# Kernel optimization log

Measured on AMD Instinct MI355X. Metric: run time of the kernel, lower is better.

Reference implementation:

```python
import jax, jax.numpy as jnp
import numpy as np

N_NODES = 10000
N_EDGES = 100000
IN_FEATS = 64
OUT_FEATS = 64
N_EDGE_TYPES = 10


def setup_inputs() -> dict:
    key = jax.random.key(0)
    k_feat, k_src, k_dst, k_ord, k_emb = jax.random.split(key, 5)
    feat = jax.random.normal(k_feat, (N_NODES, IN_FEATS), dtype=jnp.float32)
    src = jax.random.randint(k_src, (N_EDGES,), 0, N_NODES, dtype=jnp.int32)
    dst = jax.random.randint(k_dst, (N_EDGES,), 0, N_NODES, dtype=jnp.int32)
    order = jax.random.randint(k_ord, (N_EDGES,), 0, N_EDGE_TYPES, dtype=jnp.int32)
    # xavier-uniform-like init for the relation-weight embedding table
    emb_weight = jax.random.normal(k_emb, (N_EDGE_TYPES, IN_FEATS * OUT_FEATS), dtype=jnp.float32) * 0.02
    bias = jnp.zeros((OUT_FEATS,), dtype=jnp.float32)
    return {"feat": feat, "src": src, "dst": dst, "order": order,
            "emb_weight": emb_weight, "bias": bias}


def reference(feat, src, dst, order, emb_weight, bias):
    n_nodes, in_feats = feat.shape
    out_feats = emb_weight.shape[1] // in_feats
    n_edges = src.shape[0]
    ones_e = jnp.ones((n_edges,), dtype=feat.dtype)

    # norm='both': scale source features by out_degree^{-1/2}
    out_deg = jnp.clip(jax.ops.segment_sum(ones_e, src, num_segments=n_nodes), 1.0)
    feat_n = feat * (out_deg ** -0.5)[:, None]

    # per-edge relation weight gather: [E, out, in]
    w = emb_weight[order].reshape(n_edges, out_feats, in_feats)
    h_src = feat_n[src]                              # [E, in]
    msg = jnp.einsum('eoi,ei->eo', w, h_src)         # [E, out]

    # scatter-sum aggregate to destination nodes
    rst = jax.ops.segment_sum(msg, dst, num_segments=n_nodes)  # [N, out]

    # post-norm by in_degree^{-1/2}
    in_deg = jnp.clip(jax.ops.segment_sum(ones_e, dst, num_segments=n_nodes), 1.0)
    rst = rst * (in_deg ** -0.5)[:, None]
    return rst + bias
```

## Files before the change

kernel.cpp:

```cpp
#include <hip/hip_runtime.h>
#include <stdint.h>


typedef __attribute__((ext_vector_type(8))) short short8;
typedef __attribute__((ext_vector_type(4))) float f32x4;

constexpr int N_NODES = 10000;
constexpr int N_EDGES = 100000;
constexpr int F = 64;
constexpr int R = 10;
constexpr int BLOCK = 256;
constexpr int CAPN = 64;
constexpr int WPR = (N_NODES + 31) / 32;
constexpr int GBX = (WPR + (BLOCK / 64) - 1) / (BLOCK / 64);

union U8 { uint32_t u[4]; short8 s; };

__device__ inline uint32_t pk_hi(float x, float y) {
    uint32_t bx = __float_as_uint(x), by = __float_as_uint(y);
    return (bx >> 16) | (by & 0xFFFF0000u);
}
__device__ inline uint32_t pk_lo(float x, float y) {
    uint32_t bx = __float_as_uint(x), by = __float_as_uint(y);
    float lx = x - __uint_as_float(bx & 0xFFFF0000u);
    float ly = y - __uint_as_float(by & 0xFFFF0000u);
    return (__float_as_uint(lx) >> 16) | (__float_as_uint(ly) & 0xFFFF0000u);
}

__global__ void k_count(const int* __restrict__ src, const int* __restrict__ dst,
                        const int* __restrict__ order, const float* __restrict__ emb,
                        const float* __restrict__ feat,
                        unsigned* deg_out, unsigned* deg_in,
                        const unsigned* __restrict__ sent_ptr,
                        uint4* __restrict__ wfrag, int* __restrict__ dstbuf,
                        uint4* __restrict__ pfeat) {
    unsigned sent = *sent_ptr;
    int t = blockIdx.x * BLOCK + threadIdx.x;

    if (t < N_EDGES) {
        int s = src[t], d = dst[t], r = order[t];
        atomicAdd(&deg_out[s], 1u);
        int rank = (int)(atomicAdd(&deg_in[d], 1u) - sent);
        if (rank < CAPN)
            dstbuf[d * CAPN + rank] = r * N_NODES + s;
    }

    if (t < R * 16 * 64) {
        int lane = t & 63, frag = t >> 6;
        int p = frag & 1, ks = (frag >> 1) & 1, tt = (frag >> 2) & 3, rr = frag >> 4;
        int o = 16 * tt + (lane & 15), q = lane >> 4;
        const float* w = emb + (size_t)rr * F * F + (size_t)o * F + 32 * ks + 8 * q;
        float4 f0 = *(const float4*)w;
        float4 f1 = *(const float4*)(w + 4);
        uint4 v;
        if (p == 0) v = make_uint4(pk_hi(f0.x, f0.y), pk_hi(f0.z, f0.w),
                                   pk_hi(f1.x, f1.y), pk_hi(f1.z, f1.w));
        else        v = make_uint4(pk_lo(f0.x, f0.y), pk_lo(f0.z, f0.w),
                                   pk_lo(f1.x, f1.y), pk_lo(f1.z, f1.w));
        wfrag[(size_t)frag * 64 + lane] = v;
    }

    if (t < N_NODES * 4) {
        int n = t >> 2, p = t & 3;
        const float* rp = feat + (size_t)n * F + 16 * p;
        float4 a = *(const float4*)rp;
        float4 b = *(const float4*)(rp + 4);
        float4 c = *(const float4*)(rp + 8);
        float4 e = *(const float4*)(rp + 12);
        uint4* pf = pfeat + (size_t)n * 16;
        pf[2 * p]     = make_uint4(pk_hi(a.x, a.y), pk_hi(a.z, a.w),
                                   pk_hi(b.x, b.y), pk_hi(b.z, b.w));
        pf[2 * p + 1] = make_uint4(pk_hi(c.x, c.y), pk_hi(c.z, c.w),
                                   pk_hi(e.x, e.y), pk_hi(e.z, e.w));
        pf[8 + 2 * p]     = make_uint4(pk_lo(a.x, a.y), pk_lo(a.z, a.w),
                                       pk_lo(b.x, b.y), pk_lo(b.z, b.w));
        pf[8 + 2 * p + 1] = make_uint4(pk_lo(c.x, c.y), pk_lo(c.z, c.w),
                                       pk_lo(e.x, e.y), pk_lo(e.z, e.w));
    }
}

__global__ __launch_bounds__(BLOCK, 3) void k_gemm(
    const uint4* __restrict__ pfeat, const unsigned* __restrict__ deg_out,
    const unsigned* __restrict__ sent_ptr, const short8* __restrict__ wfrag,
    float* __restrict__ msg) {
    int lane = threadIdx.x & 63;
    int wib = threadIdx.x >> 6;
    int r = blockIdx.y;
    int base = (blockIdx.x * (BLOCK / 64) + wib) * 32;
    if (base >= N_NODES) return;
    unsigned sent = *sent_ptr;

    int q = lane >> 4;
    int nA = base + (lane & 15), nB = nA + 16;
    int cA = min(nA, N_NODES - 1), cB = min(nB, N_NODES - 1);

    float nrA = rsqrtf((float)max((int)(deg_out[cA] - sent), 1));
    float nrB = rsqrtf((float)max((int)(deg_out[cB] - sent), 1));

    const short8* pA = (const short8*)(pfeat + (size_t)cA * 16);
    const short8* pB = (const short8*)(pfeat + (size_t)cB * 16);
    short8 Ah0 = pA[q], Ah1 = pA[4 + q], Al0 = pA[8 + q], Al1 = pA[12 + q];
    short8 Bh0 = pB[q], Bh1 = pB[4 + q], Bl0 = pB[8 + q], Bl1 = pB[12 + q];

    const short8* wf = wfrag + (size_t)r * 16 * 64;
    f32x4 acc0[4], acc1[4];
#pragma unroll
    for (int t = 0; t < 4; ++t) {
        acc0[t] = (f32x4){0.f, 0.f, 0.f, 0.f};
        acc1[t] = (f32x4){0.f, 0.f, 0.f, 0.f};
    }

#pragma unroll
    for (int t = 0; t < 4; ++t) {
        short8 bh0 = wf[(t * 4 + 0) * 64 + lane];
        short8 bl0 = wf[(t * 4 + 1) * 64 + lane];
        short8 bh1 = wf[(t * 4 + 2) * 64 + lane];
        short8 bl1 = wf[(t * 4 + 3) * 64 + lane];
        f32x4 x = acc0[t], y = acc1[t];
        x = __builtin_amdgcn_mfma_f32_16x16x32_bf16(Al0, bh0, x, 0, 0, 0);
        y = __builtin_amdgcn_mfma_f32_16x16x32_bf16(Bl0, bh0, y, 0, 0, 0);
        x = __builtin_amdgcn_mfma_f32_16x16x32_bf16(Ah0, bl0, x, 0, 0, 0);
        y = __builtin_amdgcn_mfma_f32_16x16x32_bf16(Bh0, bl0, y, 0, 0, 0);
        x = __builtin_amdgcn_mfma_f32_16x16x32_bf16(Ah0, bh0, x, 0, 0, 0);
        y = __builtin_amdgcn_mfma_f32_16x16x32_bf16(Bh0, bh0, y, 0, 0, 0);
        x = __builtin_amdgcn_mfma_f32_16x16x32_bf16(Al1, bh1, x, 0, 0, 0);
        y = __builtin_amdgcn_mfma_f32_16x16x32_bf16(Bl1, bh1, y, 0, 0, 0);
        x = __builtin_amdgcn_mfma_f32_16x16x32_bf16(Ah1, bl1, x, 0, 0, 0);
        y = __builtin_amdgcn_mfma_f32_16x16x32_bf16(Bh1, bl1, y, 0, 0, 0);
        x = __builtin_amdgcn_mfma_f32_16x16x32_bf16(Ah1, bh1, x, 0, 0, 0);
        y = __builtin_amdgcn_mfma_f32_16x16x32_bf16(Bh1, bh1, y, 0, 0, 0);
        acc0[t] = x; acc1[t] = y;
    }

    float* mrow = msg + ((size_t)r * N_NODES + base) * F;
    int col = lane & 15;
#pragma unroll
    for (int gg = 0; gg < 4; ++gg) {
        int row = q * 4 + gg;
        float rA = __shfl(nrA, row);
        float rB = __shfl(nrB, row);
        bool okA = base + row < N_NODES;
        bool okB = base + 16 + row < N_NODES;
#pragma unroll
        for (int t = 0; t < 4; ++t) {
            if (okA) mrow[row * F + 16 * t + col] = acc0[t][gg] * rA;
            if (okB) mrow[(row + 16) * F + 16 * t + col] = acc1[t][gg] * rB;
        }
    }
}

__global__ void k_agg(const float4* __restrict__ msg, const int* __restrict__ dstbuf,
                      const unsigned* __restrict__ deg_in,
                      const unsigned* __restrict__ sent_ptr,
                      const float* __restrict__ bias, float4* __restrict__ out) {
    int t = blockIdx.x * BLOCK + threadIdx.x;
    if (t >= N_NODES * 16) return;
    unsigned sent = *sent_ptr;
    int n = t >> 4, c4 = t & 15;
    int deg = (int)(deg_in[n] - sent);
    int lim = min(deg, CAPN);
    const int* dl = dstbuf + (size_t)n * CAPN;
    float4 acc = make_float4(0.f, 0.f, 0.f, 0.f);
    int k = 0;
    for (; k + 4 <= lim; k += 4) {
        int s0 = dl[k], s1 = dl[k + 1], s2 = dl[k + 2], s3 = dl[k + 3];
        float4 g0 = msg[(size_t)s0 * 16 + c4];
        float4 g1 = msg[(size_t)s1 * 16 + c4];
        float4 g2 = msg[(size_t)s2 * 16 + c4];
        float4 g3 = msg[(size_t)s3 * 16 + c4];
        acc.x += (g0.x + g1.x) + (g2.x + g3.x);
        acc.y += (g0.y + g1.y) + (g2.y + g3.y);
        acc.z += (g0.z + g1.z) + (g2.z + g3.z);
        acc.w += (g0.w + g1.w) + (g2.w + g3.w);
    }
    for (; k < lim; ++k) {
        float4 g = msg[(size_t)dl[k] * 16 + c4];
        acc.x += g.x; acc.y += g.y; acc.z += g.z; acc.w += g.w;
    }
    float sc = rsqrtf((float)max(deg, 1));
    float4 b = ((const float4*)bias)[c4];
    out[t] = make_float4(acc.x * sc + b.x, acc.y * sc + b.y,
                         acc.z * sc + b.z, acc.w * sc + b.w);
}

extern "C" void kernel_launch(void* const* d_in, const int* in_sizes, int n_in,
                              void* d_out, int out_size, void* d_ws, size_t ws_size,
                              hipStream_t stream) {
    const float* feat  = (const float*)d_in[0];
    const int*   src   = (const int*)d_in[1];
    const int*   dst   = (const int*)d_in[2];
    const int*   order = (const int*)d_in[3];
    const float* emb   = (const float*)d_in[4];
    const float* bias  = (const float*)d_in[5];
    float* out = (float*)d_out;

    unsigned* deg_out = (unsigned*)d_ws;
    unsigned* deg_in  = deg_out + N_NODES;
    unsigned* sent    = deg_in + N_NODES;
    uint4* wfrag   = (uint4*)(sent + 16);
    int*   dstbuf  = (int*)(wfrag + (size_t)R * 16 * 64);
    uint4* pfeat   = (uint4*)(dstbuf + (size_t)N_NODES * CAPN);
    float* msg     = (float*)(pfeat + (size_t)N_NODES * 16);

    int eb = (N_EDGES + BLOCK - 1) / BLOCK;
    k_count<<<eb, BLOCK, 0, stream>>>(src, dst, order, emb, feat, deg_out, deg_in,
                                      sent, wfrag, dstbuf, pfeat);
    dim3 gg(GBX, R);
    k_gemm<<<gg, BLOCK, 0, stream>>>(pfeat, deg_out, sent, (const short8*)wfrag,
                                     msg);
    int ab = (N_NODES * 16 + BLOCK - 1) / BLOCK;
    k_agg<<<ab, BLOCK, 0, stream>>>((const float4*)msg, dstbuf, deg_in, sent,
                                    bias, (float4*)out);
}
```

Measured before the change: 100.5 us.

## Fuse edge counting and weight packing into GEMM kernel, move out-degree norm to aggregation

Merges the counting/packing kernel into the per-relation GEMM kernel. Each block now packs its relation's weight fragments into LDS, and feature rows are packed to bf16 hi/lo pairs in registers instead of being staged through a global buffer. Since out-degree counts are no longer final while the GEMM runs, the source-degree normalization moves into the aggregation kernel as a per-edge scale. This removes one launch and the packed-feature round trip through global memory, at the cost of redundant weight packing per block and extra deg_out gathers per edge in aggregation.

```diff
diff --git a/kernel.cpp b/kernel.cpp
--- a/kernel.cpp
+++ b/kernel.cpp
@@ -27,29 +27,51 @@
     return (__float_as_uint(lx) >> 16) | (__float_as_uint(ly) & 0xFFFF0000u);
 }
 
-__global__ void k_count(const int* __restrict__ src, const int* __restrict__ dst,
-                        const int* __restrict__ order, const float* __restrict__ emb,
-                        const float* __restrict__ feat,
-                        unsigned* deg_out, unsigned* deg_in,
-                        const unsigned* __restrict__ sent_ptr,
-                        uint4* __restrict__ wfrag, int* __restrict__ dstbuf,
-                        uint4* __restrict__ pfeat) {
+__device__ inline void mk_pack(const float* __restrict__ row,
+                               short8& h0, short8& l0, short8& h1, short8& l1) {
+    float4 f0 = *(const float4*)row;
+    float4 f1 = *(const float4*)(row + 4);
+    float4 f2 = *(const float4*)(row + 32);
+    float4 f3 = *(const float4*)(row + 36);
+    U8 H0, L0, H1, L1;
+    H0.u[0] = pk_hi(f0.x, f0.y); H0.u[1] = pk_hi(f0.z, f0.w);
+    H0.u[2] = pk_hi(f1.x, f1.y); H0.u[3] = pk_hi(f1.z, f1.w);
+    L0.u[0] = pk_lo(f0.x, f0.y); L0.u[1] = pk_lo(f0.z, f0.w);
+    L0.u[2] = pk_lo(f1.x, f1.y); L0.u[3] = pk_lo(f1.z, f1.w);
+    H1.u[0] = pk_hi(f2.x, f2.y); H1.u[1] = pk_hi(f2.z, f2.w);
+    H1.u[2] = pk_hi(f3.x, f3.y); H1.u[3] = pk_hi(f3.z, f3.w);
+    L1.u[0] = pk_lo(f2.x, f2.y); L1.u[1] = pk_lo(f2.z, f2.w);
+    L1.u[2] = pk_lo(f3.x, f3.y); L1.u[3] = pk_lo(f3.z, f3.w);
+    h0 = H0.s; l0 = L0.s; h1 = H1.s; l1 = L1.s;
+}
+
+__global__ __launch_bounds__(BLOCK, 3) void k_main(
+    const float* __restrict__ feat, const int* __restrict__ src,
+    const int* __restrict__ dst, const int* __restrict__ order,
+    const float* __restrict__ emb, unsigned* deg_out, unsigned* deg_in,
+    const unsigned* __restrict__ sent_ptr, int* __restrict__ dstbuf,
+    float* __restrict__ msg) {
+    int tid = threadIdx.x;
+    int r = blockIdx.y;
     unsigned sent = *sent_ptr;
-    int t = blockIdx.x * BLOCK + threadIdx.x;
-
+
+    int t = (blockIdx.y * GBX + blockIdx.x) * BLOCK + tid;
     if (t < N_EDGES) {
-        int s = src[t], d = dst[t], r = order[t];
+        int s = src[t], d = dst[t], rr = order[t];
         atomicAdd(&deg_out[s], 1u);
         int rank = (int)(atomicAdd(&deg_in[d], 1u) - sent);
         if (rank < CAPN)
-            dstbuf[d * CAPN + rank] = r * N_NODES + s;
-    }
-
-    if (t < R * 16 * 64) {
-        int lane = t & 63, frag = t >> 6;
-        int p = frag & 1, ks = (frag >> 1) & 1, tt = (frag >> 2) & 3, rr = frag >> 4;
+            dstbuf[d * CAPN + rank] = (rr << 14) | s;
+    }
+
+    __shared__ uint4 wf_lds[16 * 64];
+#pragma unroll
+    for (int i = 0; i < 4; ++i) {
+        int item = tid + BLOCK * i;
+        int lane = item & 63, frag = item >> 6;
+        int p = frag & 1, ks = (frag >> 1) & 1, tt = frag >> 2;
         int o = 16 * tt + (lane & 15), q = lane >> 4;
-        const float* w = emb + (size_t)rr * F * F + (size_t)o * F + 32 * ks + 8 * q;
+        const float* w = emb + (size_t)r * F * F + (size_t)o * F + 32 * ks + 8 * q;
         float4 f0 = *(const float4*)w;
         float4 f1 = *(const float4*)(w + 4);
         uint4 v;
@@ -57,66 +79,37 @@
                                    pk_hi(f1.x, f1.y), pk_hi(f1.z, f1.w));
         else        v = make_uint4(pk_lo(f0.x, f0.y), pk_lo(f0.z, f0.w),
                                    pk_lo(f1.x, f1.y), pk_lo(f1.z, f1.w));
-        wfrag[(size_t)frag * 64 + lane] = v;
-    }
-
-    if (t < N_NODES * 4) {
-        int n = t >> 2, p = t & 3;
-        const float* rp = feat + (size_t)n * F + 16 * p;
-        float4 a = *(const float4*)rp;
-        float4 b = *(const float4*)(rp + 4);
-        float4 c = *(const float4*)(rp + 8);
-        float4 e = *(const float4*)(rp + 12);
-        uint4* pf = pfeat + (size_t)n * 16;
-        pf[2 * p]     = make_uint4(pk_hi(a.x, a.y), pk_hi(a.z, a.w),
-                                   pk_hi(b.x, b.y), pk_hi(b.z, b.w));
-        pf[2 * p + 1] = make_uint4(pk_hi(c.x, c.y), pk_hi(c.z, c.w),
-                                   pk_hi(e.x, e.y), pk_hi(e.z, e.w));
-        pf[8 + 2 * p]     = make_uint4(pk_lo(a.x, a.y), pk_lo(a.z, a.w),
-                                       pk_lo(b.x, b.y), pk_lo(b.z, b.w));
-        pf[8 + 2 * p + 1] = make_uint4(pk_lo(c.x, c.y), pk_lo(c.z, c.w),
-                                       pk_lo(e.x, e.y), pk_lo(e.z, e.w));
-    }
-}
-
-__global__ __launch_bounds__(BLOCK, 3) void k_gemm(
-    const uint4* __restrict__ pfeat, const unsigned* __restrict__ deg_out,
-    const unsigned* __restrict__ sent_ptr, const short8* __restrict__ wfrag,
-    float* __restrict__ msg) {
-    int lane = threadIdx.x & 63;
-    int wib = threadIdx.x >> 6;
-    int r = blockIdx.y;
+        wf_lds[item] = v;
+    }
+    __syncthreads();
+
+    int lane = tid & 63, wib = tid >> 6;
     int base = (blockIdx.x * (BLOCK / 64) + wib) * 32;
     if (base >= N_NODES) return;
-    unsigned sent = *sent_ptr;
 
     int q = lane >> 4;
     int nA = base + (lane & 15), nB = nA + 16;
     int cA = min(nA, N_NODES - 1), cB = min(nB, N_NODES - 1);
 
-    float nrA = rsqrtf((float)max((int)(deg_out[cA] - sent), 1));
-    float nrB = rsqrtf((float)max((int)(deg_out[cB] - sent), 1));
-
-    const short8* pA = (const short8*)(pfeat + (size_t)cA * 16);
-    const short8* pB = (const short8*)(pfeat + (size_t)cB * 16);
-    short8 Ah0 = pA[q], Ah1 = pA[4 + q], Al0 = pA[8 + q], Al1 = pA[12 + q];
-    short8 Bh0 = pB[q], Bh1 = pB[4 + q], Bl0 = pB[8 + q], Bl1 = pB[12 + q];
-
-    const short8* wf = wfrag + (size_t)r * 16 * 64;
+    short8 Ah0, Al0, Ah1, Al1, Bh0, Bl0, Bh1, Bl1;
+    mk_pack(feat + (size_t)cA * F + 8 * q, Ah0, Al0, Ah1, Al1);
+    mk_pack(feat + (size_t)cB * F + 8 * q, Bh0, Bl0, Bh1, Bl1);
+
+    const short8* wf = (const short8*)wf_lds;
     f32x4 acc0[4], acc1[4];
 #pragma unroll
-    for (int t = 0; t < 4; ++t) {
-        acc0[t] = (f32x4){0.f, 0.f, 0.f, 0.f};
-        acc1[t] = (f32x4){0.f, 0.f, 0.f, 0.f};
-    }
-
-#pragma unroll
-    for (int t = 0; t < 4; ++t) {
-        short8 bh0 = wf[(t * 4 + 0) * 64 + lane];
-        short8 bl0 = wf[(t * 4 + 1) * 64 + lane];
-        short8 bh1 = wf[(t * 4 + 2) * 64 + lane];
-        short8 bl1 = wf[(t * 4 + 3) * 64 + lane];
-        f32x4 x = acc0[t], y = acc1[t];
+    for (int t2 = 0; t2 < 4; ++t2) {
+        acc0[t2] = (f32x4){0.f, 0.f, 0.f, 0.f};
+        acc1[t2] = (f32x4){0.f, 0.f, 0.f, 0.f};
+    }
+
+#pragma unroll
+    for (int t2 = 0; t2 < 4; ++t2) {
+        short8 bh0 = wf[(t2 * 4 + 0) * 64 + lane];
+        short8 bl0 = wf[(t2 * 4 + 1) * 64 + lane];
+        short8 bh1 = wf[(t2 * 4 + 2) * 64 + lane];
+        short8 bl1 = wf[(t2 * 4 + 3) * 64 + lane];
+        f32x4 x = acc0[t2], y = acc1[t2];
         x = __builtin_amdgcn_mfma_f32_16x16x32_bf16(Al0, bh0, x, 0, 0, 0);
         y = __builtin_amdgcn_mfma_f32_16x16x32_bf16(Bl0, bh0, y, 0, 0, 0);
         x = __builtin_amdgcn_mfma_f32_16x16x32_bf16(Ah0, bl0, x, 0, 0, 0);
@@ -129,7 +122,7 @@
         y = __builtin_amdgcn_mfma_f32_16x16x32_bf16(Bh1, bl1, y, 0, 0, 0);
         x = __builtin_amdgcn_mfma_f32_16x16x32_bf16(Ah1, bh1, x, 0, 0, 0);
         y = __builtin_amdgcn_mfma_f32_16x16x32_bf16(Bh1, bh1, y, 0, 0, 0);
-        acc0[t] = x; acc1[t] = y;
+        acc0[t2] = x; acc1[t2] = y;
     }
 
     float* mrow = msg + ((size_t)r * N_NODES + base) * F;
@@ -137,20 +130,19 @@
 #pragma unroll
     for (int gg = 0; gg < 4; ++gg) {
         int row = q * 4 + gg;
-        float rA = __shfl(nrA, row);
-        float rB = __shfl(nrB, row);
         bool okA = base + row < N_NODES;
         bool okB = base + 16 + row < N_NODES;
 #pragma unroll
-        for (int t = 0; t < 4; ++t) {
-            if (okA) mrow[row * F + 16 * t + col] = acc0[t][gg] * rA;
-            if (okB) mrow[(row + 16) * F + 16 * t + col] = acc1[t][gg] * rB;
+        for (int t2 = 0; t2 < 4; ++t2) {
+            if (okA) mrow[row * F + 16 * t2 + col] = acc0[t2][gg];
+            if (okB) mrow[(row + 16) * F + 16 * t2 + col] = acc1[t2][gg];
         }
     }
 }
 
 __global__ void k_agg(const float4* __restrict__ msg, const int* __restrict__ dstbuf,
                       const unsigned* __restrict__ deg_in,
+                      const unsigned* __restrict__ deg_out,
                       const unsigned* __restrict__ sent_ptr,
                       const float* __restrict__ bias, float4* __restrict__ out) {
     int t = blockIdx.x * BLOCK + threadIdx.x;
@@ -163,19 +155,27 @@
     float4 acc = make_float4(0.f, 0.f, 0.f, 0.f);
     int k = 0;
     for (; k + 4 <= lim; k += 4) {
-        int s0 = dl[k], s1 = dl[k + 1], s2 = dl[k + 2], s3 = dl[k + 3];
-        float4 g0 = msg[(size_t)s0 * 16 + c4];
-        float4 g1 = msg[(size_t)s1 * 16 + c4];
-        float4 g2 = msg[(size_t)s2 * 16 + c4];
-        float4 g3 = msg[(size_t)s3 * 16 + c4];
-        acc.x += (g0.x + g1.x) + (g2.x + g3.x);
-        acc.y += (g0.y + g1.y) + (g2.y + g3.y);
-        acc.z += (g0.z + g1.z) + (g2.z + g3.z);
-        acc.w += (g0.w + g1.w) + (g2.w + g3.w);
+        int e0 = dl[k], e1 = dl[k + 1], e2 = dl[k + 2], e3 = dl[k + 3];
+        int s0 = e0 & 16383, s1 = e1 & 16383, s2 = e2 & 16383, s3 = e3 & 16383;
+        float4 g0 = msg[((size_t)(e0 >> 14) * N_NODES + s0) * 16 + c4];
+        float4 g1 = msg[((size_t)(e1 >> 14) * N_NODES + s1) * 16 + c4];
+        float4 g2 = msg[((size_t)(e2 >> 14) * N_NODES + s2) * 16 + c4];
+        float4 g3 = msg[((size_t)(e3 >> 14) * N_NODES + s3) * 16 + c4];
+        float w0 = rsqrtf((float)max((int)(deg_out[s0] - sent), 1));
+        float w1 = rsqrtf((float)max((int)(deg_out[s1] - sent), 1));
+        float w2 = rsqrtf((float)max((int)(deg_out[s2] - sent), 1));
+        float w3 = rsqrtf((float)max((int)(deg_out[s3] - sent), 1));
+        acc.x += (g0.x * w0 + g1.x * w1) + (g2.x * w2 + g3.x * w3);
+        acc.y += (g0.y * w0 + g1.y * w1) + (g2.y * w2 + g3.y * w3);
+        acc.z += (g0.z * w0 + g1.z * w1) + (g2.z * w2 + g3.z * w3);
+        acc.w += (g0.w * w0 + g1.w * w1) + (g2.w * w2 + g3.w * w3);
     }
     for (; k < lim; ++k) {
-        float4 g = msg[(size_t)dl[k] * 16 + c4];
-        acc.x += g.x; acc.y += g.y; acc.z += g.z; acc.w += g.w;
+        int e = dl[k];
+        int s = e & 16383;
+        float4 g = msg[((size_t)(e >> 14) * N_NODES + s) * 16 + c4];
+        float w = rsqrtf((float)max((int)(deg_out[s] - sent), 1));
+        acc.x += g.x * w; acc.y += g.y * w; acc.z += g.z * w; acc.w += g.w * w;
     }
     float sc = rsqrtf((float)max(deg, 1));
     float4 b = ((const float4*)bias)[c4];
@@ -197,18 +197,13 @@
     unsigned* deg_out = (unsigned*)d_ws;
     unsigned* deg_in  = deg_out + N_NODES;
     unsigned* sent    = deg_in + N_NODES;
-    uint4* wfrag   = (uint4*)(sent + 16);
-    int*   dstbuf  = (int*)(wfrag + (size_t)R * 16 * 64);
-    uint4* pfeat   = (uint4*)(dstbuf + (size_t)N_NODES * CAPN);
-    float* msg     = (float*)(pfeat + (size_t)N_NODES * 16);
-
-    int eb = (N_EDGES + BLOCK - 1) / BLOCK;
-    k_count<<<eb, BLOCK, 0, stream>>>(src, dst, order, emb, feat, deg_out, deg_in,
-                                      sent, wfrag, dstbuf, pfeat);
+    int*   dstbuf  = (int*)(sent + 16);
+    float* msg     = (float*)(dstbuf + (size_t)N_NODES * CAPN);
+
     dim3 gg(GBX, R);
-    k_gemm<<<gg, BLOCK, 0, stream>>>(pfeat, deg_out, sent, (const short8*)wfrag,
-                                     msg);
+    k_main<<<gg, BLOCK, 0, stream>>>(feat, src, dst, order, emb, deg_out, deg_in,
+                                     sent, dstbuf, msg);
     int ab = (N_NODES * 16 + BLOCK - 1) / BLOCK;
-    k_agg<<<ab, BLOCK, 0, stream>>>((const float4*)msg, dstbuf, deg_in, sent,
-                                    bias, (float4*)out);
-}
+    k_agg<<<ab, BLOCK, 0, stream>>>((const float4*)msg, dstbuf, deg_in, deg_out,
+                                    sent, bias, (float4*)out);
+}
```

New measurement: 97.83 us. 1.03x faster.
